# Kernel optimization log

Hardware: AMD Instinct MI355X
Metric: run time of the kernel (lower is better)

The kernel has to match this reference:

```python
import jax, jax.numpy as jnp
from jax import lax
import numpy as np

GROUPS1 = 8  # channels // 32 for channels=256

def _conv1d(x, w, groups):
    # x: [B,C,L], w: [Cout, Cin/groups, K], padding 'same' for K=3
    return lax.conv_general_dilated(
        x, w, window_strides=(1,), padding=[(1, 1)],
        feature_group_count=groups,
        dimension_numbers=('NCH', 'OIH', 'NCH'))


def setup_inputs() -> dict:
    key = jax.random.key(0)
    ks = jax.random.split(key, 6)
    B, C, H, W = 2, 256, 512, 512
    feat = jax.random.normal(ks[0], (B, C, H, W), dtype=jnp.float32)
    w1 = jax.random.normal(ks[1], (C, C // GROUPS1, 3), dtype=jnp.float32) * 0.05
    b1 = jax.random.normal(ks[2], (C,), dtype=jnp.float32) * 0.05
    w2 = jax.random.normal(ks[3], (C, C, 3), dtype=jnp.float32) * 0.02
    b2 = jax.random.normal(ks[4], (C,), dtype=jnp.float32) * 0.05
    w_blur = jax.random.normal(ks[5], (C, 1, 3, 3), dtype=jnp.float32) * 0.1
    return {"feat": feat, "w1": w1, "b1": b1, "w2": w2, "b2": b2, "w_blur": w_blur}


def reference(feat, w1, b1, w2, b2, w_blur):
    B, C, H, W = feat.shape
    L = min(H, W)
    # diagonal gather: [B,C,L]
    diag = jnp.diagonal(feat, axis1=2, axis2=3)
    # grouped conv1d + exact GELU
    x = _conv1d(diag, w1, GROUPS1) + b1[None, :, None]
    x = jax.nn.gelu(x, approximate=False)
    # dense conv1d + exact GELU
    x = _conv1d(x, w2, 1) + b2[None, :, None]
    x = jax.nn.gelu(x, approximate=False)
    # diag_embed: scatter 1D signal onto diagonal of [B,C,H,W] (H==W==L here)
    idx = jnp.arange(L)
    dmap = jnp.zeros((B, C, L, L), dtype=feat.dtype).at[:, :, idx, idx].set(x)
    # depthwise 3x3 blur, no bias
    out = lax.conv_general_dilated(
        dmap, w_blur, window_strides=(1, 1), padding=[(1, 1), (1, 1)],
        feature_group_count=C,
        dimension_numbers=('NCHW', 'OIHW', 'NCHW'))
    return out
```

## Files before the change

kernel.cpp:

```cpp
#include <hip/hip_runtime.h>
#include <math.h>

#define BB 2
#define CC 256
#define LL 512

#define N4       33554432
#define A_QUADS  11184896
#define B_QUADS  22369792
#define ZBLK     43691
#define K3_FUSED 43690
#define ROWS_LO  174764
#define BANDBLK  683

typedef float v4f __attribute__((ext_vector_type(4)));

__device__ __forceinline__ float gelu_exact(float x) {
    return 0.5f * x * (1.0f + erff(x * 0.70710678118654752f));
}

__global__ __launch_bounds__(256) void k1(
    const float* __restrict__ feat, const float* __restrict__ w1,
    const float* __restrict__ b1, const float* __restrict__ w2,
    float* __restrict__ x1, float* __restrict__ w2t, v4f* __restrict__ out)
{
    const int tid = threadIdx.x;
    const int blk = blockIdx.x;
    if (blk >= 1024) {
        int idx4 = (blk - 1024) * 256 + tid;
        __builtin_nontemporal_store((v4f)(0.f), &out[idx4]);
        return;
    }
    if (blk < 256) {
        __shared__ float sg[32][34];
        int b  = blk >> 7;
        int g  = (blk >> 4) & 7;
        int l0 = (blk & 15) << 5;
        for (int t = tid; t < 32 * 34; t += 256) {
            int ch = t / 34;
            int j  = t - ch * 34;
            int l  = l0 + j - 1;
            int c  = (g << 5) + ch;
            sg[ch][j] = (l >= 0 && l < LL) ? feat[((b * CC + c) * LL + l) * LL + l] : 0.f;
        }
        __syncthreads();
        int ll = tid & 31;
        int os = tid >> 5;
        float a0[4] = {0.f, 0.f, 0.f, 0.f};
        float a1[4] = {0.f, 0.f, 0.f, 0.f};
        float a2[4] = {0.f, 0.f, 0.f, 0.f};
        const float* wbase = w1 + ((g << 5) + (os << 2)) * 96;
        #pragma unroll
        for (int i = 0; i < 32; ++i) {
            float dm = sg[i][ll];
            float d0 = sg[i][ll + 1];
            float dp = sg[i][ll + 2];
            #pragma unroll
            for (int it = 0; it < 4; ++it) {
                const float* wp = wbase + it * 96 + i * 3;
                a0[it] += dm * wp[0];
                a1[it] += d0 * wp[1];
                a2[it] += dp * wp[2];
            }
        }
        int l = l0 + ll;
        #pragma unroll
        for (int it = 0; it < 4; ++it) {
            int o = (g << 5) + (os << 2) + it;
            x1[((b * CC + o) << 9) + l] = gelu_exact(a0[it] + a1[it] + a2[it] + b1[o]);
        }
    } else {
        int idx = ((blk - 256) << 8) + tid;
        int o  = idx / 768;
        int ck = idx - o * 768;
        w2t[ck * CC + o] = w2[idx];
    }
}

__global__ __launch_bounds__(256) void k2(
    const float* __restrict__ x1, const float* __restrict__ w2t,
    const float* __restrict__ b2, float* __restrict__ x2, v4f* __restrict__ out)
{
    const int tid = threadIdx.x;
    const int blk = blockIdx.x;
    if (blk >= 512) {
        int idx4 = A_QUADS + (blk - 512) * 256 + tid;
        __builtin_nontemporal_store((v4f)(0.f), &out[idx4]);
        return;
    }
    __shared__ float s[CC][10];
    int oc = blk & 3;
    int lt = (blk >> 2) & 63;
    int b  = blk >> 8;
    int l0 = lt << 3;
    for (int t = tid; t < CC * 10; t += 256) {
        int c = t / 10;
        int j = t - c * 10;
        int p = l0 + j - 1;
        s[c][j] = (p >= 0 && p < LL) ? x1[((b * CC + c) << 9) + p] : 0.0f;
    }
    __syncthreads();
    int o  = (oc << 6) + (tid & 63);
    int jg = tid >> 6;
    float bias = b2[o];
    float acc0 = bias, acc1 = bias;
    const float* wp = w2t + o;
    #pragma unroll 4
    for (int c = 0; c < CC; ++c) {
        float w0  = wp[c * 768];
        float w1v = wp[c * 768 + 256];
        float w2v = wp[c * 768 + 512];
        float s0 = s[c][jg * 2 + 0];
        float s1 = s[c][jg * 2 + 1];
        float s2 = s[c][jg * 2 + 2];
        float s3 = s[c][jg * 2 + 3];
        acc0 += s0 * w0 + s1 * w1v + s2 * w2v;
        acc1 += s1 * w0 + s2 * w1v + s3 * w2v;
    }
    int l = l0 + jg * 2;
    float* xo = x2 + ((b * CC + o) << 9) + l;
    xo[0] = gelu_exact(acc0);
    xo[1] = gelu_exact(acc1);
}

__global__ __launch_bounds__(256) void k3(
    const float* __restrict__ x2, const float* __restrict__ wb,
    float* __restrict__ outf, v4f* __restrict__ out)
{
    const int tid = threadIdx.x;
    const int blk = blockIdx.x;
    if (blk < BANDBLK) {
        int row = blk * 256 + tid;
        if (row >= ROWS_LO) return;
        int i  = row & (LL - 1);
        int bc = row >> 9;
        const float* xr = x2 + (bc << 9);
        float xm = (i > 0)      ? xr[i - 1] : 0.f;
        float x0 = xr[i];
        float xp = (i < LL - 1) ? xr[i + 1] : 0.f;
        const float* w = wb + (bc & (CC - 1)) * 9;
        float v0 = w[2] * xm;
        float v1 = w[1] * xm + w[5] * x0;
        float v2 = w[0] * xm + w[4] * x0 + w[8] * xp;
        float v3 = w[3] * x0 + w[7] * xp;
        float v4 = w[6] * xp;
        float* r = outf + ((long long)row << 9);
        if (i >= 2)      r[i - 2] = v0;
        if (i >= 1)      r[i - 1] = v1;
        r[i] = v2;
        if (i <= LL - 2) r[i + 1] = v3;
        if (i <= LL - 3) r[i + 2] = v4;
        return;
    }
    int idx4 = B_QUADS + (blk - BANDBLK) * 256 + tid;
    int row = idx4 >> 7;
    int i   = row & (LL - 1);
    int d0  = ((idx4 & 127) << 2) - i;
    v4f v = (v4f)(0.f);
    if ((unsigned)(d0 + 5) <= 7u) {
        int bc = row >> 9;
        const float* xr = x2 + (bc << 9);
        float xm = (i > 0)      ? xr[i - 1] : 0.f;
        float x0 = xr[i];
        float xp = (i < LL - 1) ? xr[i + 1] : 0.f;
        const float* w = wb + (bc & (CC - 1)) * 9;
        #pragma unroll
        for (int t = 0; t < 4; ++t) {
            int d = d0 + t;
            float r = 0.f;
            if (d == -2)      r = w[2] * xm;
            else if (d == -1) r = w[1] * xm + w[5] * x0;
            else if (d == 0)  r = w[0] * xm + w[4] * x0 + w[8] * xp;
            else if (d == 1)  r = w[3] * x0 + w[7] * xp;
            else if (d == 2)  r = w[6] * xp;
            v[t] = r;
        }
    }
    __builtin_nontemporal_store(v, &out[idx4]);
}

extern "C" void kernel_launch(void* const* d_in, const int* in_sizes, int n_in,
                              void* d_out, int out_size, void* d_ws, size_t ws_size,
                              hipStream_t stream) {
    const float* feat   = (const float*)d_in[0];
    const float* w1     = (const float*)d_in[1];
    const float* b1     = (const float*)d_in[2];
    const float* w2     = (const float*)d_in[3];
    const float* b2     = (const float*)d_in[4];
    const float* w_blur = (const float*)d_in[5];
    float* ws = (float*)d_ws;

    const int N = BB * CC * LL;
    float* x1  = ws;
    float* x2  = ws + N;
    float* w2t = ws + 2 * N;

    k1<<<1024 + ZBLK, 256, 0, stream>>>(feat, w1, b1, w2, x1, w2t, (v4f*)d_out);
    k2<<<512 + ZBLK, 256, 0, stream>>>(x1, w2t, b2, x2, (v4f*)d_out);
    k3<<<BANDBLK + K3_FUSED, 256, 0, stream>>>(x2, w_blur, (float*)d_out, (v4f*)d_out);
}
```

Baseline: 146.0 us.

## Fuse dense conv1d with diagonal blur scatter and move zero-fill into first kernel

The second conv1d kernel now computes a halo of extra outputs in shared memory and applies the depthwise 3x3 blur itself, writing the five-wide band straight into the output. This removes the third kernel and the x2 intermediate buffer. The whole zero-fill of the output moves into k1 instead of being spread across all three launches. In exchange, k2 does extra halo arithmetic, all band writes become scattered scalar stores issued after the full zero-fill, and k2's compute can no longer overlap with zero-fill blocks.

```diff
diff --git a/kernel.cpp b/kernel.cpp
--- a/kernel.cpp
+++ b/kernel.cpp
@@ -4,14 +4,7 @@
 #define BB 2
 #define CC 256
 #define LL 512
-
-#define N4       33554432
-#define A_QUADS  11184896
-#define B_QUADS  22369792
-#define ZBLK     43691
-#define K3_FUSED 43690
-#define ROWS_LO  174764
-#define BANDBLK  683
+#define N4 33554432
 
 typedef float v4f __attribute__((ext_vector_type(4)));
 
@@ -79,104 +72,77 @@
 
 __global__ __launch_bounds__(256) void k2(
     const float* __restrict__ x1, const float* __restrict__ w2t,
-    const float* __restrict__ b2, float* __restrict__ x2, v4f* __restrict__ out)
+    const float* __restrict__ b2, const float* __restrict__ wb,
+    float* __restrict__ out)
 {
+    __shared__ float s1[CC][14];
+    __shared__ float s2[64][13];
     const int tid = threadIdx.x;
     const int blk = blockIdx.x;
-    if (blk >= 512) {
-        int idx4 = A_QUADS + (blk - 512) * 256 + tid;
-        __builtin_nontemporal_store((v4f)(0.f), &out[idx4]);
-        return;
-    }
-    __shared__ float s[CC][10];
     int oc = blk & 3;
     int lt = (blk >> 2) & 63;
     int b  = blk >> 8;
     int l0 = lt << 3;
-    for (int t = tid; t < CC * 10; t += 256) {
-        int c = t / 10;
-        int j = t - c * 10;
-        int p = l0 + j - 1;
-        s[c][j] = (p >= 0 && p < LL) ? x1[((b * CC + c) << 9) + p] : 0.0f;
+
+    for (int t = tid; t < CC * 14; t += 256) {
+        int c = t / 14;
+        int j = t - c * 14;
+        int p = l0 + j - 3;
+        s1[c][j] = (p >= 0 && p < LL) ? x1[((b * CC + c) << 9) + p] : 0.0f;
     }
     __syncthreads();
-    int o  = (oc << 6) + (tid & 63);
+
+    int ol = tid & 63;
     int jg = tid >> 6;
+    int o  = (oc << 6) + ol;
     float bias = b2[o];
-    float acc0 = bias, acc1 = bias;
+    float acc[3];
+    #pragma unroll
+    for (int r = 0; r < 3; ++r) acc[r] = bias;
     const float* wp = w2t + o;
     #pragma unroll 4
     for (int c = 0; c < CC; ++c) {
         float w0  = wp[c * 768];
         float w1v = wp[c * 768 + 256];
         float w2v = wp[c * 768 + 512];
-        float s0 = s[c][jg * 2 + 0];
-        float s1 = s[c][jg * 2 + 1];
-        float s2 = s[c][jg * 2 + 2];
-        float s3 = s[c][jg * 2 + 3];
-        acc0 += s0 * w0 + s1 * w1v + s2 * w2v;
-        acc1 += s1 * w0 + s2 * w1v + s3 * w2v;
+        float t0 = s1[c][jg * 3 + 0];
+        float t1 = s1[c][jg * 3 + 1];
+        float t2 = s1[c][jg * 3 + 2];
+        float t3 = s1[c][jg * 3 + 3];
+        float t4 = s1[c][jg * 3 + 4];
+        acc[0] += t0 * w0 + t1 * w1v + t2 * w2v;
+        acc[1] += t1 * w0 + t2 * w1v + t3 * w2v;
+        acc[2] += t2 * w0 + t3 * w1v + t4 * w2v;
     }
-    int l = l0 + jg * 2;
-    float* xo = x2 + ((b * CC + o) << 9) + l;
-    xo[0] = gelu_exact(acc0);
-    xo[1] = gelu_exact(acc1);
-}
+    #pragma unroll
+    for (int r = 0; r < 3; ++r) {
+        int p = l0 - 2 + jg * 3 + r;
+        s2[ol][jg * 3 + r] = (p >= 0 && p < LL) ? gelu_exact(acc[r]) : 0.0f;
+    }
+    __syncthreads();
 
-__global__ __launch_bounds__(256) void k3(
-    const float* __restrict__ x2, const float* __restrict__ wb,
-    float* __restrict__ outf, v4f* __restrict__ out)
-{
-    const int tid = threadIdx.x;
-    const int blk = blockIdx.x;
-    if (blk < BANDBLK) {
-        int row = blk * 256 + tid;
-        if (row >= ROWS_LO) return;
-        int i  = row & (LL - 1);
-        int bc = row >> 9;
-        const float* xr = x2 + (bc << 9);
-        float xm = (i > 0)      ? xr[i - 1] : 0.f;
-        float x0 = xr[i];
-        float xp = (i < LL - 1) ? xr[i + 1] : 0.f;
-        const float* w = wb + (bc & (CC - 1)) * 9;
-        float v0 = w[2] * xm;
-        float v1 = w[1] * xm + w[5] * x0;
-        float v2 = w[0] * xm + w[4] * x0 + w[8] * xp;
-        float v3 = w[3] * x0 + w[7] * xp;
-        float v4 = w[6] * xp;
-        float* r = outf + ((long long)row << 9);
-        if (i >= 2)      r[i - 2] = v0;
-        if (i >= 1)      r[i - 1] = v1;
-        r[i] = v2;
-        if (i <= LL - 2) r[i + 1] = v3;
-        if (i <= LL - 3) r[i + 2] = v4;
-        return;
+    const float* w = wb + ((b ? o : o)) * 9;
+    const float* wc = wb + o * 9;
+    (void)w;
+    #pragma unroll
+    for (int r2 = 0; r2 < 2; ++r2) {
+        int i  = l0 + (jg << 1) + r2;
+        int li = (jg << 1) + r2;
+        float xm = s2[ol][li + 1];
+        float x0 = s2[ol][li + 2];
+        float xp = s2[ol][li + 3];
+        float v0 = wc[2] * xm;
+        float v1 = wc[1] * xm + wc[5] * x0;
+        float v2 = wc[0] * xm + wc[4] * x0 + wc[8] * xp;
+        float v3 = wc[3] * x0 + wc[7] * xp;
+        float v4 = wc[6] * xp;
+        float* rowp = out + (((long long)(b * CC + o) << 9) + i) * LL;
+        if (i >= 2)      rowp[i - 2] = v0;
+        if (i >= 1)      rowp[i - 1] = v1;
+        rowp[i] = v2;
+        if (i <= LL - 2) rowp[i + 1] = v3;
+        if (i <= LL - 3) rowp[i + 2] = v4;
     }
-    int idx4 = B_QUADS + (blk - BANDBLK) * 256 + tid;
-    int row = idx4 >> 7;
-    int i   = row & (LL - 1);
-    int d0  = ((idx4 & 127) << 2) - i;
-    v4f v = (v4f)(0.f);
-    if ((unsigned)(d0 + 5) <= 7u) {
-        int bc = row >> 9;
-        const float* xr = x2 + (bc << 9);
-        float xm = (i > 0)      ? xr[i - 1] : 0.f;
-        float x0 = xr[i];
-        float xp = (i < LL - 1) ? xr[i + 1] : 0.f;
-        const float* w = wb + (bc & (CC - 1)) * 9;
-        #pragma unroll
-        for (int t = 0; t < 4; ++t) {
-            int d = d0 + t;
-            float r = 0.f;
-            if (d == -2)      r = w[2] * xm;
-            else if (d == -1) r = w[1] * xm + w[5] * x0;
-            else if (d == 0)  r = w[0] * xm + w[4] * x0 + w[8] * xp;
-            else if (d == 1)  r = w[3] * x0 + w[7] * xp;
-            else if (d == 2)  r = w[6] * xp;
-            v[t] = r;
-        }
-    }
-    __builtin_nontemporal_store(v, &out[idx4]);
 }
 
 extern "C" void kernel_launch(void* const* d_in, const int* in_sizes, int n_in,
@@ -192,10 +158,8 @@
 
     const int N = BB * CC * LL;
     float* x1  = ws;
-    float* x2  = ws + N;
-    float* w2t = ws + 2 * N;
+    float* w2t = ws + N;
 
-    k1<<<1024 + ZBLK, 256, 0, stream>>>(feat, w1, b1, w2, x1, w2t, (v4f*)d_out);
-    k2<<<512 + ZBLK, 256, 0, stream>>>(x1, w2t, b2, x2, (v4f*)d_out);
-    k3<<<BANDBLK + K3_FUSED, 256, 0, stream>>>(x2, w_blur, (float*)d_out, (v4f*)d_out);
+    k1<<<1024 + N4 / 256, 256, 0, stream>>>(feat, w1, b1, w2, x1, w2t, (v4f*)d_out);
+    k2<<<512, 256, 0, stream>>>(x1, w2t, b2, w_blur, (float*)d_out);
 }
```

New measurement: 186.2 us. +27.5%, slower.

## Write banded rows as full 64-byte lines and rebalance zero-fill across kernels

Applied to the files above, without the earlier changes.

The band-only rows in k3 now write complete 16-float line segments around the diagonal with vectorized nontemporal stores, instead of scattered scalar stores into a region that was already zero-filled. The other k3 blocks skip these rows. Because the banded rows no longer need a separate zero pass, the out-buffer split between k1/k2 zero-fill and k3 is rebalanced: k1 and k2 each clear more of the output and k3 handles fewer fused blocks. The aim is to cut redundant zero writes and partial-line store traffic, at the cost of more work per band thread and a shifted load balance between the kernels.

```diff
diff --git a/kernel.cpp b/kernel.cpp
--- a/kernel.cpp
+++ b/kernel.cpp
@@ -6,12 +6,12 @@
 #define LL 512
 
 #define N4       33554432
-#define A_QUADS  11184896
-#define B_QUADS  22369792
-#define ZBLK     43691
-#define K3_FUSED 43690
-#define ROWS_LO  174764
-#define BANDBLK  683
+#define ZBLK12   48900
+#define A_QUADS  12518400
+#define B_QUADS  25036800
+#define FBLK     33272
+#define ROWS_BANDED 195600
+#define BANDBLK  765
 
 typedef float v4f __attribute__((ext_vector_type(4)));
 
@@ -125,13 +125,13 @@
 
 __global__ __launch_bounds__(256) void k3(
     const float* __restrict__ x2, const float* __restrict__ wb,
-    float* __restrict__ outf, v4f* __restrict__ out)
+    v4f* __restrict__ out)
 {
     const int tid = threadIdx.x;
     const int blk = blockIdx.x;
     if (blk < BANDBLK) {
         int row = blk * 256 + tid;
-        if (row >= ROWS_LO) return;
+        if (row >= ROWS_BANDED) return;
         int i  = row & (LL - 1);
         int bc = row >> 9;
         const float* xr = x2 + (bc << 9);
@@ -139,17 +139,36 @@
         float x0 = xr[i];
         float xp = (i < LL - 1) ? xr[i + 1] : 0.f;
         const float* w = wb + (bc & (CC - 1)) * 9;
-        float v0 = w[2] * xm;
-        float v1 = w[1] * xm + w[5] * x0;
-        float v2 = w[0] * xm + w[4] * x0 + w[8] * xp;
-        float v3 = w[3] * x0 + w[7] * xp;
-        float v4 = w[6] * xp;
-        float* r = outf + ((long long)row << 9);
-        if (i >= 2)      r[i - 2] = v0;
-        if (i >= 1)      r[i - 1] = v1;
-        r[i] = v2;
-        if (i <= LL - 2) r[i + 1] = v3;
-        if (i <= LL - 3) r[i + 2] = v4;
+        float bv[5];
+        bv[0] = w[2] * xm;
+        bv[1] = w[1] * xm + w[5] * x0;
+        bv[2] = w[0] * xm + w[4] * x0 + w[8] * xp;
+        bv[3] = w[3] * x0 + w[7] * xp;
+        bv[4] = w[6] * xp;
+        int jlo = (i >= 2) ? i - 2 : 0;
+        int jhi = (i <= LL - 3) ? i + 2 : LL - 1;
+        int Llo = jlo >> 4;
+        int Lhi = jhi >> 4;
+        int rowq = row << 7;
+        for (int L = Llo; L <= Lhi; ++L) {
+            float line[16];
+            #pragma unroll
+            for (int t = 0; t < 16; ++t) line[t] = 0.f;
+            int base = L << 4;
+            #pragma unroll
+            for (int d = 0; d < 5; ++d) {
+                int j = i - 2 + d;
+                int t = j - base;
+                if (j >= jlo && j <= jhi && t >= 0 && t < 16) line[t] = bv[d];
+            }
+            #pragma unroll
+            for (int q = 0; q < 4; ++q) {
+                v4f v;
+                v[0] = line[q * 4 + 0]; v[1] = line[q * 4 + 1];
+                v[2] = line[q * 4 + 2]; v[3] = line[q * 4 + 3];
+                __builtin_nontemporal_store(v, &out[rowq + (L << 2) + q]);
+            }
+        }
         return;
     }
     int idx4 = B_QUADS + (blk - BANDBLK) * 256 + tid;
@@ -195,7 +214,7 @@
     float* x2  = ws + N;
     float* w2t = ws + 2 * N;
 
-    k1<<<1024 + ZBLK, 256, 0, stream>>>(feat, w1, b1, w2, x1, w2t, (v4f*)d_out);
-    k2<<<512 + ZBLK, 256, 0, stream>>>(x1, w2t, b2, x2, (v4f*)d_out);
-    k3<<<BANDBLK + K3_FUSED, 256, 0, stream>>>(x2, w_blur, (float*)d_out, (v4f*)d_out);
-}
+    k1<<<1024 + ZBLK12, 256, 0, stream>>>(feat, w1, b1, w2, x1, w2t, (v4f*)d_out);
+    k2<<<512 + ZBLK12, 256, 0, stream>>>(x1, w2t, b2, x2, (v4f*)d_out);
+    k3<<<BANDBLK + FBLK, 256, 0, stream>>>(x2, w_blur, (v4f*)d_out);
+}
```

Result: slower. 152.9 us (+4.8%).
